# Kernel optimization log

Measured on AMD Instinct MI355X. Metric: run time of the kernel, lower is better.

Reference implementation:

```python
import jax, jax.numpy as jnp
import numpy as np

NUM_LAYERS = 4

def setup_inputs() -> dict:
    key = jax.random.key(0)
    x = jax.random.normal(key, (4000000, 9), dtype=jnp.float32)
    return {"x": x}

def reference(x) -> jnp.ndarray:
    # reshape to batched 3x3 matrices
    xm = x.reshape(-1, 3, 3)
    # Frobenius norm per matrix, keepdims for broadcast
    norm = jnp.sqrt(jnp.sum(xm * xm, axis=(1, 2), keepdims=True))
    Q = xm / norm
    for _ in range(NUM_LAYERS):
        # N = Q^T Q  (b33)
        N = jnp.einsum('bji,bjk->bik', Q, Q)
        P = 0.5 * jnp.einsum('bij,bjk->bik', Q, N)
        Q = 2.0 * Q + jnp.einsum('bij,bjk->bik', P, N) - 3.0 * P
    return Q.reshape(x.shape)
```

## Files before the change

### kernel.cpp

```cpp
#include <hip/hip_runtime.h>


#define NLAYERS 4

typedef float v4f __attribute__((ext_vector_type(4)));
typedef const __attribute__((address_space(1))) v4f gv4f_t;
typedef __attribute__((address_space(3))) v4f lv4f_t;

__global__ __launch_bounds__(256, 8) void
proj_kernel(const float* __restrict__ x, float* __restrict__ out) {
    __shared__ float lin[256 * 9];
    __shared__ float lout[256 * 9];
    const int tid = threadIdx.x;
    const long long mbase = (long long)blockIdx.x * 256;

    const v4f* __restrict__ gin = (const v4f*)(x + mbase * 9);
    v4f* lin4 = (v4f*)lin;
    const int wslot = tid & ~63;
    __builtin_amdgcn_global_load_lds((gv4f_t*)(gin + tid),
                                     (lv4f_t*)(lin4 + wslot), 16, 0, 0);
    __builtin_amdgcn_global_load_lds((gv4f_t*)(gin + 256 + tid),
                                     (lv4f_t*)(lin4 + 256 + wslot), 16, 0, 0);
    if (tid < 64)
        __builtin_amdgcn_global_load_lds((gv4f_t*)(gin + 512 + tid),
                                         (lv4f_t*)(lin4 + 512), 16, 0, 0);
    __syncthreads();

    float q[9];
#pragma unroll
    for (int k = 0; k < 9; ++k) q[k] = lin[tid * 9 + k];

    float s = 0.f;
#pragma unroll
    for (int k = 0; k < 9; ++k) s = __builtin_fmaf(q[k], q[k], s);
    const float inv = rsqrtf(s);
#pragma unroll
    for (int k = 0; k < 9; ++k) q[k] *= inv;

#pragma unroll
    for (int layer = 0; layer < NLAYERS; ++layer) {
        const float n00 = q[0]*q[0] + q[3]*q[3] + q[6]*q[6];
        const float n01 = q[0]*q[1] + q[3]*q[4] + q[6]*q[7];
        const float n02 = q[0]*q[2] + q[3]*q[5] + q[6]*q[8];
        const float n11 = q[1]*q[1] + q[4]*q[4] + q[7]*q[7];
        const float n12 = q[1]*q[2] + q[4]*q[5] + q[7]*q[8];
        const float n22 = q[2]*q[2] + q[5]*q[5] + q[8]*q[8];

        const float a00 = __builtin_fmaf(0.5f, n00, -1.5f);
        const float a11 = __builtin_fmaf(0.5f, n11, -1.5f);
        const float a22 = __builtin_fmaf(0.5f, n22, -1.5f);
        const float a01 = 0.5f * n01;
        const float a02 = 0.5f * n02;
        const float a12 = 0.5f * n12;

        const float m00 = __builtin_fmaf(a00,n00, __builtin_fmaf(a01,n01, __builtin_fmaf(a02,n02, 2.0f)));
        const float m01 = __builtin_fmaf(a00,n01, __builtin_fmaf(a01,n11, a02*n12));
        const float m02 = __builtin_fmaf(a00,n02, __builtin_fmaf(a01,n12, a02*n22));
        const float m11 = __builtin_fmaf(a01,n01, __builtin_fmaf(a11,n11, __builtin_fmaf(a12,n12, 2.0f)));
        const float m12 = __builtin_fmaf(a01,n02, __builtin_fmaf(a11,n12, a12*n22));
        const float m22 = __builtin_fmaf(a02,n02, __builtin_fmaf(a12,n12, __builtin_fmaf(a22,n22, 2.0f)));

        float qn[9];
#pragma unroll
        for (int i = 0; i < 3; ++i) {
            const float q0 = q[3*i], q1 = q[3*i+1], q2 = q[3*i+2];
            qn[3*i+0] = __builtin_fmaf(q0, m00, __builtin_fmaf(q1, m01, q2 * m02));
            qn[3*i+1] = __builtin_fmaf(q0, m01, __builtin_fmaf(q1, m11, q2 * m12));
            qn[3*i+2] = __builtin_fmaf(q0, m02, __builtin_fmaf(q1, m12, q2 * m22));
        }
#pragma unroll
        for (int k = 0; k < 9; ++k) q[k] = qn[k];
    }

#pragma unroll
    for (int k = 0; k < 9; ++k) lout[tid * 9 + k] = q[k];
    __syncthreads();

    v4f* __restrict__ gout = (v4f*)(out + mbase * 9);
    const v4f* lout4 = (const v4f*)lout;
    __builtin_nontemporal_store(lout4[tid],       gout + tid);
    __builtin_nontemporal_store(lout4[tid + 256], gout + tid + 256);
    if (tid < 64)
        __builtin_nontemporal_store(lout4[tid + 512], gout + tid + 512);
}

extern "C" void kernel_launch(void* const* d_in, const int* in_sizes, int n_in,
                              void* d_out, int out_size, void* d_ws, size_t ws_size,
                              hipStream_t stream) {
    const float* x = (const float*)d_in[0];
    float* out = (float*)d_out;
    const int nmat = in_sizes[0] / 9;
    const int blocks = nmat / 256;
    proj_kernel<<<blocks, 256, 0, stream>>>(x, out);
}
```

Baseline: 247.7 us.

## Use persistent per-wave grid-stride loop with register prefetch and double-buffered LDS

Replaces one-block-per-256-matrices with a fixed grid of 2048 blocks in which each wave processes 64-matrix tiles in a grid-stride loop. The next tile's global loads are issued into registers before computing the current tile, then written to a second LDS buffer, so memory latency overlaps compute. Block-wide barriers are dropped in favour of wave-private LDS regions. This adds register pressure and loop overhead, and gives up the direct global-to-LDS loads and the high block count used for latency hiding.

```diff
diff --git a/kernel.cpp b/kernel.cpp
--- a/kernel.cpp
+++ b/kernel.cpp
@@ -2,86 +2,116 @@
 
 
 #define NLAYERS 4
+#define GRID_BLOCKS 2048
+#define WPB 4
+#define TOTAL_WAVES (GRID_BLOCKS * WPB)
+#define WFLOATS 576
 
 typedef float v4f __attribute__((ext_vector_type(4)));
-typedef const __attribute__((address_space(1))) v4f gv4f_t;
-typedef __attribute__((address_space(3))) v4f lv4f_t;
 
 __global__ __launch_bounds__(256, 8) void
-proj_kernel(const float* __restrict__ x, float* __restrict__ out) {
-    __shared__ float lin[256 * 9];
-    __shared__ float lout[256 * 9];
-    const int tid = threadIdx.x;
-    const long long mbase = (long long)blockIdx.x * 256;
+proj_kernel(const float* __restrict__ x, float* __restrict__ out, int nwt) {
+    __shared__ float lds[2][WPB][WFLOATS];
+    const int tid  = threadIdx.x;
+    const int lane = tid & 63;
+    const int w    = tid >> 6;
+    const int gw   = blockIdx.x * WPB + w;
 
-    const v4f* __restrict__ gin = (const v4f*)(x + mbase * 9);
-    v4f* lin4 = (v4f*)lin;
-    const int wslot = tid & ~63;
-    __builtin_amdgcn_global_load_lds((gv4f_t*)(gin + tid),
-                                     (lv4f_t*)(lin4 + wslot), 16, 0, 0);
-    __builtin_amdgcn_global_load_lds((gv4f_t*)(gin + 256 + tid),
-                                     (lv4f_t*)(lin4 + 256 + wslot), 16, 0, 0);
-    if (tid < 64)
-        __builtin_amdgcn_global_load_lds((gv4f_t*)(gin + 512 + tid),
-                                         (lv4f_t*)(lin4 + 512), 16, 0, 0);
-    __syncthreads();
+    const int n = (nwt - gw + TOTAL_WAVES - 1) / TOTAL_WAVES;
+    if (n <= 0) return;
 
-    float q[9];
+    float* cur = &lds[0][w][0];
+    float* nxt = &lds[1][w][0];
+
+    {
+        const v4f* g4 = (const v4f*)(x + (long long)gw * WFLOATS);
+        v4f r0 = g4[lane];
+        v4f r1 = g4[lane + 64];
+        v4f r2;
+        if (lane < 16) r2 = g4[lane + 128];
+        v4f* l4 = (v4f*)cur;
+        l4[lane]      = r0;
+        l4[lane + 64] = r1;
+        if (lane < 16) l4[lane + 128] = r2;
+    }
+
+    for (int k = 0; k < n; ++k) {
+        const long long t = gw + (long long)k * TOTAL_WAVES;
+        const bool has_next = (k + 1 < n);
+
+        v4f p0, p1, p2;
+        if (has_next) {
+            const v4f* g4n = (const v4f*)(x + (t + TOTAL_WAVES) * WFLOATS);
+            p0 = g4n[lane];
+            p1 = g4n[lane + 64];
+            if (lane < 16) p2 = g4n[lane + 128];
+        }
+
+        float q[9];
 #pragma unroll
-    for (int k = 0; k < 9; ++k) q[k] = lin[tid * 9 + k];
+        for (int j = 0; j < 9; ++j) q[j] = cur[lane * 9 + j];
 
-    float s = 0.f;
+        float s = 0.f;
 #pragma unroll
-    for (int k = 0; k < 9; ++k) s = __builtin_fmaf(q[k], q[k], s);
-    const float inv = rsqrtf(s);
+        for (int j = 0; j < 9; ++j) s = __builtin_fmaf(q[j], q[j], s);
+        const float inv = rsqrtf(s);
 #pragma unroll
-    for (int k = 0; k < 9; ++k) q[k] *= inv;
+        for (int j = 0; j < 9; ++j) q[j] *= inv;
 
 #pragma unroll
-    for (int layer = 0; layer < NLAYERS; ++layer) {
-        const float n00 = q[0]*q[0] + q[3]*q[3] + q[6]*q[6];
-        const float n01 = q[0]*q[1] + q[3]*q[4] + q[6]*q[7];
-        const float n02 = q[0]*q[2] + q[3]*q[5] + q[6]*q[8];
-        const float n11 = q[1]*q[1] + q[4]*q[4] + q[7]*q[7];
-        const float n12 = q[1]*q[2] + q[4]*q[5] + q[7]*q[8];
-        const float n22 = q[2]*q[2] + q[5]*q[5] + q[8]*q[8];
+        for (int layer = 0; layer < NLAYERS; ++layer) {
+            const float n00 = q[0]*q[0] + q[3]*q[3] + q[6]*q[6];
+            const float n01 = q[0]*q[1] + q[3]*q[4] + q[6]*q[7];
+            const float n02 = q[0]*q[2] + q[3]*q[5] + q[6]*q[8];
+            const float n11 = q[1]*q[1] + q[4]*q[4] + q[7]*q[7];
+            const float n12 = q[1]*q[2] + q[4]*q[5] + q[7]*q[8];
+            const float n22 = q[2]*q[2] + q[5]*q[5] + q[8]*q[8];
 
-        const float a00 = __builtin_fmaf(0.5f, n00, -1.5f);
-        const float a11 = __builtin_fmaf(0.5f, n11, -1.5f);
-        const float a22 = __builtin_fmaf(0.5f, n22, -1.5f);
-        const float a01 = 0.5f * n01;
-        const float a02 = 0.5f * n02;
-        const float a12 = 0.5f * n12;
+            const float a00 = __builtin_fmaf(0.5f, n00, -1.5f);
+            const float a11 = __builtin_fmaf(0.5f, n11, -1.5f);
+            const float a22 = __builtin_fmaf(0.5f, n22, -1.5f);
+            const float a01 = 0.5f * n01;
+            const float a02 = 0.5f * n02;
+            const float a12 = 0.5f * n12;
 
-        const float m00 = __builtin_fmaf(a00,n00, __builtin_fmaf(a01,n01, __builtin_fmaf(a02,n02, 2.0f)));
-        const float m01 = __builtin_fmaf(a00,n01, __builtin_fmaf(a01,n11, a02*n12));
-        const float m02 = __builtin_fmaf(a00,n02, __builtin_fmaf(a01,n12, a02*n22));
-        const float m11 = __builtin_fmaf(a01,n01, __builtin_fmaf(a11,n11, __builtin_fmaf(a12,n12, 2.0f)));
-        const float m12 = __builtin_fmaf(a01,n02, __builtin_fmaf(a11,n12, a12*n22));
-        const float m22 = __builtin_fmaf(a02,n02, __builtin_fmaf(a12,n12, __builtin_fmaf(a22,n22, 2.0f)));
+            const float m00 = __builtin_fmaf(a00,n00, __builtin_fmaf(a01,n01, __builtin_fmaf(a02,n02, 2.0f)));
+            const float m01 = __builtin_fmaf(a00,n01, __builtin_fmaf(a01,n11, a02*n12));
+            const float m02 = __builtin_fmaf(a00,n02, __builtin_fmaf(a01,n12, a02*n22));
+            const float m11 = __builtin_fmaf(a01,n01, __builtin_fmaf(a11,n11, __builtin_fmaf(a12,n12, 2.0f)));
+            const float m12 = __builtin_fmaf(a01,n02, __builtin_fmaf(a11,n12, a12*n22));
+            const float m22 = __builtin_fmaf(a02,n02, __builtin_fmaf(a12,n12, __builtin_fmaf(a22,n22, 2.0f)));
 
-        float qn[9];
+            float qn[9];
 #pragma unroll
-        for (int i = 0; i < 3; ++i) {
-            const float q0 = q[3*i], q1 = q[3*i+1], q2 = q[3*i+2];
-            qn[3*i+0] = __builtin_fmaf(q0, m00, __builtin_fmaf(q1, m01, q2 * m02));
-            qn[3*i+1] = __builtin_fmaf(q0, m01, __builtin_fmaf(q1, m11, q2 * m12));
-            qn[3*i+2] = __builtin_fmaf(q0, m02, __builtin_fmaf(q1, m12, q2 * m22));
+            for (int i = 0; i < 3; ++i) {
+                const float q0 = q[3*i], q1 = q[3*i+1], q2 = q[3*i+2];
+                qn[3*i+0] = __builtin_fmaf(q0, m00, __builtin_fmaf(q1, m01, q2 * m02));
+                qn[3*i+1] = __builtin_fmaf(q0, m01, __builtin_fmaf(q1, m11, q2 * m12));
+                qn[3*i+2] = __builtin_fmaf(q0, m02, __builtin_fmaf(q1, m12, q2 * m22));
+            }
+#pragma unroll
+            for (int j = 0; j < 9; ++j) q[j] = qn[j];
         }
-#pragma unroll
-        for (int k = 0; k < 9; ++k) q[k] = qn[k];
-    }
 
 #pragma unroll
-    for (int k = 0; k < 9; ++k) lout[tid * 9 + k] = q[k];
-    __syncthreads();
+        for (int j = 0; j < 9; ++j) cur[lane * 9 + j] = q[j];
+        {
+            const v4f* l4 = (const v4f*)cur;
+            v4f* g4 = (v4f*)(out + t * WFLOATS);
+            __builtin_nontemporal_store(l4[lane],      g4 + lane);
+            __builtin_nontemporal_store(l4[lane + 64], g4 + lane + 64);
+            if (lane < 16)
+                __builtin_nontemporal_store(l4[lane + 128], g4 + lane + 128);
+        }
 
-    v4f* __restrict__ gout = (v4f*)(out + mbase * 9);
-    const v4f* lout4 = (const v4f*)lout;
-    __builtin_nontemporal_store(lout4[tid],       gout + tid);
-    __builtin_nontemporal_store(lout4[tid + 256], gout + tid + 256);
-    if (tid < 64)
-        __builtin_nontemporal_store(lout4[tid + 512], gout + tid + 512);
+        if (has_next) {
+            v4f* l4n = (v4f*)nxt;
+            l4n[lane]      = p0;
+            l4n[lane + 64] = p1;
+            if (lane < 16) l4n[lane + 128] = p2;
+            float* tmp = cur; cur = nxt; nxt = tmp;
+        }
+    }
 }
 
 extern "C" void kernel_launch(void* const* d_in, const int* in_sizes, int n_in,
@@ -90,6 +120,6 @@
     const float* x = (const float*)d_in[0];
     float* out = (float*)d_out;
     const int nmat = in_sizes[0] / 9;
-    const int blocks = nmat / 256;
-    proj_kernel<<<blocks, 256, 0, stream>>>(x, out);
+    const int nwt = nmat / 64;
+    proj_kernel<<<GRID_BLOCKS, 256, 0, stream>>>(x, out, nwt);
 }
```

Result: no change. 249.8 us (+0.8%).
